# Performance work log

Hardware: AMD Instinct MI355X
Metric: run time of the kernel (lower is better)

Reference implementation:

```python
import jax, jax.numpy as jnp
import numpy as np

N = 1024
DIM = 128
HEADS = 8
DK = DIM // HEADS
EDIM = 16
EPS = 1e-5
NEG = -10000.0


def _lin(k, din, dout):
    return jax.random.normal(k, (din, dout), jnp.float32) * (1.0 / np.sqrt(din))


def setup_inputs() -> dict:
    key = jax.random.key(0)
    ks = jax.random.split(key, 10)
    mask = jax.random.randint(ks[2], (N, N), 0, 2).astype(bool)
    mask = mask | jnp.eye(N, dtype=bool)  # self-loops always valid
    return {
        "x": jax.random.normal(ks[0], (N, DIM), jnp.float32),
        "edge_feat": jax.random.normal(ks[1], (N, N, EDIM), jnp.float32),
        "mask": mask,
        "Wq": _lin(ks[3], DIM, DIM), "bq": jnp.zeros((DIM,), jnp.float32),
        "Wk": _lin(ks[4], DIM, DIM), "bk": jnp.zeros((DIM,), jnp.float32),
        "Wv": _lin(ks[5], DIM, DIM), "bv": jnp.zeros((DIM,), jnp.float32),
        "Wae": _lin(ks[6], EDIM, HEADS), "bae": jnp.zeros((HEADS,), jnp.float32),
        "Wve": _lin(ks[7], EDIM, DIM), "bve": jnp.zeros((DIM,), jnp.float32),
        "Wo": _lin(ks[8], DIM, DIM), "bo": jnp.zeros((DIM,), jnp.float32),
        "gamma": jnp.ones((DIM,), jnp.float32),
        "beta": jnp.zeros((DIM,), jnp.float32),
    }


def reference(x, edge_feat, mask, Wq, bq, Wk, bk, Wv, bv, Wae, bae, Wve, bve, Wo, bo, gamma, beta):
    n, dim = x.shape
    heads = bae.shape[0]
    dk = dim // heads
    # pre-LayerNorm
    mu = jnp.mean(x, axis=-1, keepdims=True)
    var = jnp.mean(jnp.square(x - mu), axis=-1, keepdims=True)
    h = (x - mu) * jax.lax.rsqrt(var + EPS) * gamma + beta
    q = (h @ Wq + bq).reshape(n, heads, dk)
    k = (h @ Wk + bk).reshape(n, heads, dk)
    v = (h @ Wv + bv).reshape(n, heads, dk)
    # attention logits with per-edge additive bias: (n, m, heads)
    att = jnp.einsum('nhd,mhd->nmh', q, k) / np.sqrt(dk).astype(np.float32)
    att = att + edge_feat @ Wae + bae
    att = jnp.where(mask[..., None], att, NEG)
    alpha = jax.nn.softmax(att, axis=1)  # softmax over source nodes m
    # edge-conditioned values: msg_{nm} = v_m + U(e_{nm})
    edge_val = (edge_feat @ Wve + bve).reshape(n, n, heads, dk)
    out = jnp.einsum('nmh,mhd->nhd', alpha, v) + jnp.einsum('nmh,nmhd->nhd', alpha, edge_val)
    out = out.reshape(n, dim) @ Wo + bo
    return x + out
```

## Files before the change

### kernel.cpp

```cpp
#include <hip/hip_runtime.h>
#include <hip/hip_bf16.h>

#define NNODE 1024
#define DIM 128
#define HEADS 8
#define DK 16
#define EDIM 16
#define BN 8
#define NGRP 8
#define LOG2E 1.44269504f

#define PAR 1536
#define WREG (2 * PAR)
#define SMEM_F (4 * WREG)

__global__ __launch_bounds__(384)
void ln_qkv_kernel(const float* __restrict__ x,
                   const float* __restrict__ Wq, const float* __restrict__ bq,
                   const float* __restrict__ Wk, const float* __restrict__ bk,
                   const float* __restrict__ Wv, const float* __restrict__ bv,
                   const float* __restrict__ gamma, const float* __restrict__ beta,
                   float* __restrict__ qg, float* __restrict__ kg, float* __restrict__ vg) {
    const int n = blockIdx.x;
    const int t = threadIdx.x;
    __shared__ float hrow[DIM];
    __shared__ float part[4];

    float xv = 0.f;
    if (t < 128) {
        xv = x[n * DIM + t];
        float v = xv;
        #pragma unroll
        for (int off = 32; off >= 1; off >>= 1) v += __shfl_xor(v, off);
        if ((t & 63) == 0) part[t >> 6] = v;
    }
    __syncthreads();
    const float mu = (part[0] + part[1]) * (1.0f / DIM);
    const float dx = xv - mu;
    if (t < 128) {
        float v = dx * dx;
        #pragma unroll
        for (int off = 32; off >= 1; off >>= 1) v += __shfl_xor(v, off);
        if ((t & 63) == 0) part[2 + (t >> 6)] = v;
    }
    __syncthreads();
    if (t < 128) {
        const float var = (part[2] + part[3]) * (1.0f / DIM);
        hrow[t] = dx * rsqrtf(var + 1e-5f) * gamma[t] + beta[t];
    }
    __syncthreads();

    const int which = t >> 7;
    const int col = t & 127;
    const float* W = (which == 0) ? Wq : (which == 1) ? Wk : Wv;
    const float* b = (which == 0) ? bq : (which == 1) ? bk : bv;
    float* o       = (which == 0) ? qg : (which == 1) ? kg : vg;
    float a0 = b[col], a1 = 0.f;
    #pragma unroll 8
    for (int i = 0; i < DIM; i += 2) {
        a0 = fmaf(hrow[i],     W[i * DIM + col],       a0);
        a1 = fmaf(hrow[i + 1], W[(i + 1) * DIM + col], a1);
    }
    o[n * DIM + col] = a0 + a1;
}

__device__ __forceinline__ void gll16(const float* g, float* l) {
    auto* gp = (const __attribute__((address_space(1))) unsigned int*)(g);
    auto* lp = (__attribute__((address_space(3))) unsigned int*)(l);
    __builtin_amdgcn_global_load_lds(gp, lp, 16, 0, 0);
}

__global__ __launch_bounds__(256, 1)
void attn_kernel(const float* __restrict__ qg, const float* __restrict__ kg,
                 const float* __restrict__ vg, const float* __restrict__ ef,
                 const int* __restrict__ mask,
                 const float* __restrict__ Wae, const float* __restrict__ bae,
                 float* __restrict__ acc) {
    const int t = threadIdx.x;
    const int lane = t & 63;
    const int wid = t >> 6;
    const int sp = lane >> 5;
    const int np = (lane >> 3) & 3;
    const int h  = lane & 7;
    const int bx = blockIdx.x;
    const int n0  = (bx >> 3) * BN;
    const int grp = bx & 7;
    const int mb_w = grp * 128 + wid * 32;

    __shared__ float smem[SMEM_F];
    float* wreg = smem + wid * WREG;

    float qreg[2][DK];
    #pragma unroll
    for (int hf = 0; hf < 2; ++hf) {
        const float* qp = qg + (size_t)(n0 + np + 4 * hf) * DIM + h * DK;
        #pragma unroll
        for (int d4 = 0; d4 < 4; ++d4) {
            const float4 qv = *(const float4*)(qp + d4 * 4);
            qreg[hf][d4 * 4 + 0] = qv.x; qreg[hf][d4 * 4 + 1] = qv.y;
            qreg[hf][d4 * 4 + 2] = qv.z; qreg[hf][d4 * 4 + 3] = qv.w;
        }
    }
    float waec[EDIM];
    #pragma unroll
    for (int e = 0; e < EDIM; ++e) waec[e] = Wae[e * HEADS + h] * LOG2E;
    const float baeh = bae[h] * LOG2E;

    float sl[2] = {0.f, 0.f};
    float accv[2][DK], accT[2][EDIM];
    #pragma unroll
    for (int hf = 0; hf < 2; ++hf) {
        #pragma unroll
        for (int d = 0; d < DK; ++d) accv[hf][d] = 0.f;
        #pragma unroll
        for (int e = 0; e < EDIM; ++e) accT[hf][e] = 0.f;
    }

    const int s0   = lane & 3;
    const int h0   = (lane >> 2) & 7;
    const int row0 = lane >> 5;
    const int koff = row0 * 128 + h0 * 16 + (((s0 - (h0 >> 1)) & 3) << 2);
    const float* ks0 = kg + (size_t)mb_w * 128 + koff;
    const float* ks1 = ks0 + 256;
    const float* vs0 = vg + (size_t)mb_w * 128 + koff;
    const float* vs1 = vs0 + 256;
    const int nn0 = lane >> 4;
    const int ml0 = (lane >> 2) & 3;
    const float* es0 = ef + ((size_t)(n0 + nn0) * NNODE + mb_w + ml0) * EDIM
                          + (((s0 - nn0) & 3) << 2);
    const float* es1 = es0 + (size_t)4 * NNODE * EDIM;
    const int* mp0 = mask + (size_t)(n0 + np) * NNODE + mb_w + 2 * sp;
    const int* mp1 = mp0 + (size_t)4 * NNODE;

    int krot[4], erot[4];
    const int rotk = (h >> 1) & 3;
    #pragma unroll
    for (int i = 0; i < 4; ++i) {
        krot[i] = ((i + rotk) & 3) << 2;
        erot[i] = ((i + np) & 3) << 2;
    }

    asm volatile("s_waitcnt vmcnt(0)" ::: "memory");

    int2 mkA[2], mkB[2];

#define ISSUE_BATCH(P, MKN)                                              \
    do {                                                                 \
        float* db = wreg + (P);                                          \
        gll16(ks0, db);        gll16(ks1, db + 256);                     \
        gll16(vs0, db + 512);  gll16(vs1, db + 768);                     \
        gll16(es0, db + 1024); gll16(es1, db + 1280);                    \
        MKN[0] = *(const int2*)mp0; MKN[1] = *(const int2*)mp1;          \
        ks0 += 512; ks1 += 512; vs0 += 512; vs1 += 512;                  \
        es0 += 64;  es1 += 64;  mp0 += 4;   mp1 += 4;                    \
    } while (0)

#define COMPUTE_CHUNK(P, MK)                                                   \
    do {                                                                       \
        const float* kl = wreg + (P) + sp * 256 + h * 16;                      \
        const float* vl = kl + 512;                                            \
        const float* el = wreg + (P) + 1024 + np * 64 + sp * 32;               \
        _Pragma("unroll")                                                      \
        for (int j = 0; j < 2; ++j) {                                          \
            float kk[DK], vv[DK];                                              \
            _Pragma("unroll")                                                  \
            for (int i = 0; i < 4; ++i) {                                      \
                const float4 k4 = *(const float4*)(kl + j * 128 + krot[i]);    \
                kk[i*4+0]=k4.x; kk[i*4+1]=k4.y; kk[i*4+2]=k4.z; kk[i*4+3]=k4.w;\
                const float4 v4 = *(const float4*)(vl + j * 128 + krot[i]);    \
                vv[i*4+0]=v4.x; vv[i*4+1]=v4.y; vv[i*4+2]=v4.z; vv[i*4+3]=v4.w;\
            }                                                                  \
            _Pragma("unroll")                                                  \
            for (int hf = 0; hf < 2; ++hf) {                                   \
                float efv[EDIM];                                               \
                _Pragma("unroll")                                              \
                for (int i = 0; i < 4; ++i) {                                  \
                    const float4 e4 =                                          \
                        *(const float4*)(el + hf * 256 + j * 16 + erot[i]);    \
                    efv[i*4+0]=e4.x; efv[i*4+1]=e4.y;                          \
                    efv[i*4+2]=e4.z; efv[i*4+3]=e4.w;                          \
                }                                                              \
                float bias = baeh, dot = 0.f;                                  \
                _Pragma("unroll")                                              \
                for (int e = 0; e < EDIM; ++e) bias = fmaf(efv[e], waec[e], bias); \
                _Pragma("unroll")                                              \
                for (int d = 0; d < DK; ++d) dot = fmaf(qreg[hf][d], kk[d], dot);  \
                const float lg = fmaf(dot, 0.25f * LOG2E, bias);               \
                const int mv = j ? MK[hf].y : MK[hf].x;                        \
                const float p = mv ? __builtin_amdgcn_exp2f(lg) : 0.f;         \
                sl[hf] += p;                                                   \
                _Pragma("unroll")                                              \
                for (int d = 0; d < DK; ++d) accv[hf][d] = fmaf(p, vv[d], accv[hf][d]); \
                _Pragma("unroll")                                              \
                for (int e = 0; e < EDIM; ++e) accT[hf][e] = fmaf(p, efv[e], accT[hf][e]); \
            }                                                                  \
        }                                                                      \
    } while (0)

    ISSUE_BATCH(0, mkA);

    #pragma unroll 1
    for (int cc = 0; cc < 8; cc += 2) {
        ISSUE_BATCH(PAR, mkB);
        asm volatile("s_waitcnt vmcnt(8)" ::: "memory");
        COMPUTE_CHUNK(0, mkA);
        if (cc < 6) {
            ISSUE_BATCH(0, mkA);
            asm volatile("s_waitcnt vmcnt(8)" ::: "memory");
        } else {
            asm volatile("s_waitcnt vmcnt(0)" ::: "memory");
        }
        COMPUTE_CHUNK(PAR, mkB);
    }
#undef ISSUE_BATCH
#undef COMPUTE_CHUNK

    #pragma unroll
    for (int hf = 0; hf < 2; ++hf) {
        sl[hf] += __shfl_xor(sl[hf], 32);
        #pragma unroll
        for (int d = 0; d < DK; ++d) accv[hf][d] += __shfl_xor(accv[hf][d], 32);
        #pragma unroll
        for (int e = 0; e < EDIM; ++e) accT[hf][e] += __shfl_xor(accT[hf][e], 32);
    }
    __syncthreads();
    float* red = smem;
    if (lane < 32) {
        float* rp = &red[((wid * 4 + np) * 8 + h) * 66];
        #pragma unroll
        for (int hf = 0; hf < 2; ++hf) {
            rp[hf * 33 + 0] = sl[hf];
            #pragma unroll
            for (int d = 0; d < DK; ++d) rp[hf * 33 + 1 + d] = accv[hf][d];
            #pragma unroll
            for (int e = 0; e < EDIM; ++e) rp[hf * 33 + 17 + e] = accT[hf][e];
        }
    }
    __syncthreads();
    for (int v = t; v < BN * HEADS * 33; v += 256) {
        const int n = v / 264;
        const int rem = v - n * 264;
        const int hh = rem / 33;
        const int idx = rem - hh * 33;
        const int nnp = n & 3, hf = n >> 2;
        float sum = 0.f;
        #pragma unroll
        for (int w = 0; w < 4; ++w)
            sum += red[((w * 4 + nnp) * 8 + hh) * 66 + hf * 33 + idx];
        acc[((size_t)(n0 + n) * NGRP + grp) * 264 + rem] = sum;
    }
}

__global__ __launch_bounds__(128)
void final_kernel(const float* __restrict__ acc,
                  const float* __restrict__ Wve, const float* __restrict__ bve,
                  const float* __restrict__ x,
                  const float* __restrict__ Wo, const float* __restrict__ bo,
                  float* __restrict__ out) {
    const int n = blockIdx.x, t = threadIdx.x;
    __shared__ float ab[HEADS * 33];
    __shared__ float orow[DIM];
    const float* ap = acc + (size_t)n * NGRP * 264;
    for (int u = t; u < HEADS * 33; u += 128) {
        float sv = 0.f;
        #pragma unroll
        for (int g = 0; g < NGRP; ++g) sv += ap[g * 264 + u];
        ab[u] = sv;
    }
    __syncthreads();
    const int col = t, hh = col >> 4, dd = col & 15;
    const float slv = ab[hh * 33];
    float acc2 = 0.f;
    #pragma unroll
    for (int e = 0; e < EDIM; ++e) acc2 = fmaf(ab[hh * 33 + 17 + e], Wve[e * DIM + col], acc2);
    orow[col] = (ab[hh * 33 + 1 + dd] + acc2) / slv + bve[col];
    __syncthreads();
    float o0 = bo[col] + x[(size_t)n * DIM + col], o1 = 0.f;
    #pragma unroll 8
    for (int i = 0; i < DIM; i += 2) {
        o0 = fmaf(orow[i],     Wo[i * DIM + col],       o0);
        o1 = fmaf(orow[i + 1], Wo[(i + 1) * DIM + col], o1);
    }
    out[(size_t)n * DIM + col] = o0 + o1;
}

extern "C" void kernel_launch(void* const* d_in, const int* in_sizes, int n_in,
                              void* d_out, int out_size, void* d_ws, size_t ws_size,
                              hipStream_t stream) {
    const float* x     = (const float*)d_in[0];
    const float* ef    = (const float*)d_in[1];
    const int*   mask  = (const int*)d_in[2];
    const float* Wq    = (const float*)d_in[3];
    const float* bq    = (const float*)d_in[4];
    const float* Wk    = (const float*)d_in[5];
    const float* bk    = (const float*)d_in[6];
    const float* Wv    = (const float*)d_in[7];
    const float* bv    = (const float*)d_in[8];
    const float* Wae   = (const float*)d_in[9];
    const float* bae   = (const float*)d_in[10];
    const float* Wve   = (const float*)d_in[11];
    const float* bve   = (const float*)d_in[12];
    const float* Wo    = (const float*)d_in[13];
    const float* bo    = (const float*)d_in[14];
    const float* gamma = (const float*)d_in[15];
    const float* beta  = (const float*)d_in[16];

    float* ws = (float*)d_ws;
    float* accb = ws;
    float* qg   = ws + (size_t)NNODE * NGRP * 264;
    float* kg   = qg + (size_t)NNODE * DIM;
    float* vg   = kg + (size_t)NNODE * DIM;

    ln_qkv_kernel<<<NNODE, 384, 0, stream>>>(x, Wq, bq, Wk, bk, Wv, bv, gamma, beta, qg, kg, vg);
    attn_kernel<<<(NNODE / BN) * NGRP, 256, 0, stream>>>(qg, kg, vg, ef, mask, Wae, bae, accb);
    final_kernel<<<NNODE, 128, 0, stream>>>(accb, Wve, bve, x, Wo, bo, (float*)d_out);
}
```

Baseline: 183.9 us.

## Pack mask to bits in QKV kernel and halve attention LDS staging for two blocks per CU

The int32 mask is packed into a bitmask inside the LN/QKV kernel, so the attention kernel loads two 32-bit words per thread instead of streaming int2 mask values every chunk. The attention pipeline now stages two source nodes per chunk instead of four. That halves the per-wave LDS buffers, and launch bounds are raised to allow two blocks per CU for more latency hiding. The trade-off is twice as many pipeline iterations and waitcnt points, smaller async loads per batch, and extra work in the first kernel.

```diff
diff --git a/kernel.cpp b/kernel.cpp
--- a/kernel.cpp
+++ b/kernel.cpp
@@ -10,9 +10,9 @@
 #define NGRP 8
 #define LOG2E 1.44269504f
 
-#define PAR 1536
+#define PAR 768
 #define WREG (2 * PAR)
-#define SMEM_F (4 * WREG)
+#define SMEM_F 8448
 
 __global__ __launch_bounds__(384)
 void ln_qkv_kernel(const float* __restrict__ x,
@@ -20,11 +20,21 @@
                    const float* __restrict__ Wk, const float* __restrict__ bk,
                    const float* __restrict__ Wv, const float* __restrict__ bv,
                    const float* __restrict__ gamma, const float* __restrict__ beta,
-                   float* __restrict__ qg, float* __restrict__ kg, float* __restrict__ vg) {
+                   const int* __restrict__ mask,
+                   float* __restrict__ qg, float* __restrict__ kg, float* __restrict__ vg,
+                   unsigned char* __restrict__ maskb) {
     const int n = blockIdx.x;
     const int t = threadIdx.x;
     __shared__ float hrow[DIM];
     __shared__ float part[4];
+
+    if (t < 128) {
+        const int* mrow = mask + (size_t)n * NNODE + t * 8;
+        unsigned pb = 0;
+        #pragma unroll
+        for (int i = 0; i < 8; ++i) pb |= (mrow[i] ? 1u : 0u) << i;
+        maskb[(size_t)n * 128 + t] = (unsigned char)pb;
+    }
 
     float xv = 0.f;
     if (t < 128) {
@@ -70,10 +80,10 @@
     __builtin_amdgcn_global_load_lds(gp, lp, 16, 0, 0);
 }
 
-__global__ __launch_bounds__(256, 1)
+__global__ __launch_bounds__(256, 2)
 void attn_kernel(const float* __restrict__ qg, const float* __restrict__ kg,
                  const float* __restrict__ vg, const float* __restrict__ ef,
-                 const int* __restrict__ mask,
+                 const unsigned char* __restrict__ maskb,
                  const float* __restrict__ Wae, const float* __restrict__ bae,
                  float* __restrict__ acc) {
     const int t = threadIdx.x;
@@ -106,6 +116,9 @@
     for (int e = 0; e < EDIM; ++e) waec[e] = Wae[e * HEADS + h] * LOG2E;
     const float baeh = bae[h] * LOG2E;
 
+    unsigned mk0 = *(const unsigned*)(maskb + (size_t)(n0 + np)     * 128 + (mb_w >> 3)) >> sp;
+    unsigned mk1 = *(const unsigned*)(maskb + (size_t)(n0 + np + 4) * 128 + (mb_w >> 3)) >> sp;
+
     float sl[2] = {0.f, 0.f};
     float accv[2][DK], accT[2][EDIM];
     #pragma unroll
@@ -119,18 +132,11 @@
     const int s0   = lane & 3;
     const int h0   = (lane >> 2) & 7;
     const int row0 = lane >> 5;
-    const int koff = row0 * 128 + h0 * 16 + (((s0 - (h0 >> 1)) & 3) << 2);
-    const float* ks0 = kg + (size_t)mb_w * 128 + koff;
-    const float* ks1 = ks0 + 256;
-    const float* vs0 = vg + (size_t)mb_w * 128 + koff;
-    const float* vs1 = vs0 + 256;
-    const int nn0 = lane >> 4;
-    const int ml0 = (lane >> 2) & 3;
-    const float* es0 = ef + ((size_t)(n0 + nn0) * NNODE + mb_w + ml0) * EDIM
-                          + (((s0 - nn0) & 3) << 2);
-    const float* es1 = es0 + (size_t)4 * NNODE * EDIM;
-    const int* mp0 = mask + (size_t)(n0 + np) * NNODE + mb_w + 2 * sp;
-    const int* mp1 = mp0 + (size_t)4 * NNODE;
+    const int koffl = row0 * 128 + h0 * 16 + (((s0 - (h0 >> 1)) & 3) << 2);
+    const int nn0 = lane >> 3;
+    const int mm0 = (lane >> 2) & 1;
+    const int eoffl = nn0 * (NNODE * EDIM) + mm0 * EDIM + (((s0 - nn0) & 3) << 2);
+    const float* efb = ef + (size_t)n0 * NNODE * EDIM;
 
     int krot[4], erot[4];
     const int rotk = (h >> 1) & 3;
@@ -140,77 +146,67 @@
         erot[i] = ((i + np) & 3) << 2;
     }
 
-    asm volatile("s_waitcnt vmcnt(0)" ::: "memory");
-
-    int2 mkA[2], mkB[2];
-
-#define ISSUE_BATCH(P, MKN)                                              \
+#define ISSUE_BATCH(DB, MB)                                              \
     do {                                                                 \
-        float* db = wreg + (P);                                          \
-        gll16(ks0, db);        gll16(ks1, db + 256);                     \
-        gll16(vs0, db + 512);  gll16(vs1, db + 768);                     \
-        gll16(es0, db + 1024); gll16(es1, db + 1280);                    \
-        MKN[0] = *(const int2*)mp0; MKN[1] = *(const int2*)mp1;          \
-        ks0 += 512; ks1 += 512; vs0 += 512; vs1 += 512;                  \
-        es0 += 64;  es1 += 64;  mp0 += 4;   mp1 += 4;                    \
+        float* db = (DB);                                                \
+        gll16(kg + (size_t)(MB) * DIM + koffl, db);                      \
+        gll16(vg + (size_t)(MB) * DIM + koffl, db + 256);                \
+        gll16(efb + (size_t)(MB) * EDIM + eoffl, db + 512);              \
     } while (0)
 
-#define COMPUTE_CHUNK(P, MK)                                                   \
+#define COMPUTE_CHUNK(DB)                                                      \
     do {                                                                       \
-        const float* kl = wreg + (P) + sp * 256 + h * 16;                      \
-        const float* vl = kl + 512;                                            \
-        const float* el = wreg + (P) + 1024 + np * 64 + sp * 32;               \
+        const float* kl = (DB) + sp * 128 + h * 16;                            \
+        const float* vl = kl + 256;                                            \
+        const float* eb = (DB) + 512 + np * 32 + sp * 16;                      \
+        float kk[DK], vv[DK];                                                  \
         _Pragma("unroll")                                                      \
-        for (int j = 0; j < 2; ++j) {                                          \
-            float kk[DK], vv[DK];                                              \
+        for (int i = 0; i < 4; ++i) {                                          \
+            const float4 k4 = *(const float4*)(kl + krot[i]);                  \
+            kk[i*4+0]=k4.x; kk[i*4+1]=k4.y; kk[i*4+2]=k4.z; kk[i*4+3]=k4.w;    \
+            const float4 v4 = *(const float4*)(vl + krot[i]);                  \
+            vv[i*4+0]=v4.x; vv[i*4+1]=v4.y; vv[i*4+2]=v4.z; vv[i*4+3]=v4.w;    \
+        }                                                                      \
+        _Pragma("unroll")                                                      \
+        for (int hf = 0; hf < 2; ++hf) {                                       \
+            float efv[EDIM];                                                   \
             _Pragma("unroll")                                                  \
             for (int i = 0; i < 4; ++i) {                                      \
-                const float4 k4 = *(const float4*)(kl + j * 128 + krot[i]);    \
-                kk[i*4+0]=k4.x; kk[i*4+1]=k4.y; kk[i*4+2]=k4.z; kk[i*4+3]=k4.w;\
-                const float4 v4 = *(const float4*)(vl + j * 128 + krot[i]);    \
-                vv[i*4+0]=v4.x; vv[i*4+1]=v4.y; vv[i*4+2]=v4.z; vv[i*4+3]=v4.w;\
+                const float4 e4 = *(const float4*)(eb + hf * 128 + erot[i]);   \
+                efv[i*4+0]=e4.x; efv[i*4+1]=e4.y;                              \
+                efv[i*4+2]=e4.z; efv[i*4+3]=e4.w;                              \
             }                                                                  \
-            _Pragma("unroll")                                                  \
-            for (int hf = 0; hf < 2; ++hf) {                                   \
-                float efv[EDIM];                                               \
-                _Pragma("unroll")                                              \
-                for (int i = 0; i < 4; ++i) {                                  \
-                    const float4 e4 =                                          \
-                        *(const float4*)(el + hf * 256 + j * 16 + erot[i]);    \
-                    efv[i*4+0]=e4.x; efv[i*4+1]=e4.y;                          \
-                    efv[i*4+2]=e4.z; efv[i*4+3]=e4.w;                          \
-                }                                                              \
-                float bias = baeh, dot = 0.f;                                  \
-                _Pragma("unroll")                                              \
-                for (int e = 0; e < EDIM; ++e) bias = fmaf(efv[e], waec[e], bias); \
-                _Pragma("unroll")                                              \
-                for (int d = 0; d < DK; ++d) dot = fmaf(qreg[hf][d], kk[d], dot);  \
-                const float lg = fmaf(dot, 0.25f * LOG2E, bias);               \
-                const int mv = j ? MK[hf].y : MK[hf].x;                        \
-                const float p = mv ? __builtin_amdgcn_exp2f(lg) : 0.f;         \
-                sl[hf] += p;                                                   \
-                _Pragma("unroll")                                              \
-                for (int d = 0; d < DK; ++d) accv[hf][d] = fmaf(p, vv[d], accv[hf][d]); \
-                _Pragma("unroll")                                              \
-                for (int e = 0; e < EDIM; ++e) accT[hf][e] = fmaf(p, efv[e], accT[hf][e]); \
-            }                                                                  \
+            float bias = baeh, dot = 0.f;                                      \
+            _Pragma("unroll")                                                  \
+            for (int e = 0; e < EDIM; ++e) bias = fmaf(efv[e], waec[e], bias); \
+            _Pragma("unroll")                                                  \
+            for (int d = 0; d < DK; ++d) dot = fmaf(qreg[hf][d], kk[d], dot);  \
+            const float lg = fmaf(dot, 0.25f * LOG2E, bias);                   \
+            const unsigned mv = (hf ? mk1 : mk0) & 1u;                         \
+            const float p = mv ? __builtin_amdgcn_exp2f(lg) : 0.f;             \
+            sl[hf] += p;                                                       \
+            _Pragma("unroll")                                                  \
+            for (int d = 0; d < DK; ++d) accv[hf][d] = fmaf(p, vv[d], accv[hf][d]); \
+            _Pragma("unroll")                                                  \
+            for (int e = 0; e < EDIM; ++e) accT[hf][e] = fmaf(p, efv[e], accT[hf][e]); \
         }                                                                      \
+        mk0 >>= 2; mk1 >>= 2;                                                  \
     } while (0)
 
-    ISSUE_BATCH(0, mkA);
+    ISSUE_BATCH(wreg, mb_w);
 
     #pragma unroll 1
-    for (int cc = 0; cc < 8; cc += 2) {
-        ISSUE_BATCH(PAR, mkB);
-        asm volatile("s_waitcnt vmcnt(8)" ::: "memory");
-        COMPUTE_CHUNK(0, mkA);
-        if (cc < 6) {
-            ISSUE_BATCH(0, mkA);
-            asm volatile("s_waitcnt vmcnt(8)" ::: "memory");
+    for (int cc = 0; cc < 16; cc += 2) {
+        ISSUE_BATCH(wreg + PAR, mb_w + 2 * (cc + 1));
+        asm volatile("s_waitcnt vmcnt(3)" ::: "memory");
+        COMPUTE_CHUNK(wreg);
+        if (cc < 14) {
+            ISSUE_BATCH(wreg, mb_w + 2 * (cc + 2));
+            asm volatile("s_waitcnt vmcnt(3)" ::: "memory");
         } else {
             asm volatile("s_waitcnt vmcnt(0)" ::: "memory");
         }
-        COMPUTE_CHUNK(PAR, mkB);
+        COMPUTE_CHUNK(wreg + PAR);
     }
 #undef ISSUE_BATCH
 #undef COMPUTE_CHUNK
@@ -310,8 +306,10 @@
     float* qg   = ws + (size_t)NNODE * NGRP * 264;
     float* kg   = qg + (size_t)NNODE * DIM;
     float* vg   = kg + (size_t)NNODE * DIM;
-
-    ln_qkv_kernel<<<NNODE, 384, 0, stream>>>(x, Wq, bq, Wk, bk, Wv, bv, gamma, beta, qg, kg, vg);
-    attn_kernel<<<(NNODE / BN) * NGRP, 256, 0, stream>>>(qg, kg, vg, ef, mask, Wae, bae, accb);
+    unsigned char* maskb = (unsigned char*)(vg + (size_t)NNODE * DIM);
+
+    ln_qkv_kernel<<<NNODE, 384, 0, stream>>>(x, Wq, bq, Wk, bk, Wv, bv, gamma, beta,
+                                             mask, qg, kg, vg, maskb);
+    attn_kernel<<<(NNODE / BN) * NGRP, 256, 0, stream>>>(qg, kg, vg, ef, maskb, Wae, bae, accb);
     final_kernel<<<NNODE, 128, 0, stream>>>(accb, Wve, bve, x, Wo, bo, (float*)d_out);
 }
```

Measured after the change: 171.4 us. 1.07x faster.
